# Performance work log

Hardware: AMD Instinct MI355X
Metric: run time of the kernel (lower is better)

Reference implementation:

```python
import jax, jax.numpy as jnp
import numpy as np

B_GRAPHS = 256      # graphs per batch
NPG = 256           # nodes per graph
EXTENT = 32.0       # coordinate extent
K1 = 5              # kernel size per dim
KK = K1 * K1        # 25 weight matrices (dim=2)


def _cartesian(pos, row, col, ev):
    # pseudo-coords: relative cartesian, globally rescaled into [0,1]
    d = pos[col] - pos[row]                                   # [E,2]
    m = jnp.max(jnp.where(ev[:, None] > 0, jnp.abs(d), 0.0))
    return d / (2.0 * m + 1e-12) + 0.5


def _spline_conv(x, row, col, pseudo, ev, W, root, bias, n):
    # degree-1 open B-spline basis, 4 nonzero corners per edge (dim=2)
    v = pseudo * (K1 - 1)
    i0 = jnp.clip(jnp.floor(v), 0, K1 - 2).astype(jnp.int32)  # [E,2]
    f = v - i0
    xin = x[col]                                              # [E,Fin] gather
    acc = jnp.zeros((n * KK, x.shape[1]), x.dtype)
    for sx in (0, 1):
        for sy in (0, 1):
            idx = (i0[:, 0] + sx) * K1 + (i0[:, 1] + sy)      # flat kernel id
            wx = f[:, 0] if sx else 1.0 - f[:, 0]
            wy = f[:, 1] if sy else 1.0 - f[:, 1]
            b = wx * wy * ev
            acc = acc.at[row * KK + idx].add(b[:, None] * xin)
    acc = acc.reshape(n, KK, x.shape[1])                      # [n,25,Fin]
    deg = jax.ops.segment_sum(ev, row, num_segments=n)
    out = jnp.einsum('nki,kio->no', acc, W) / jnp.maximum(deg, 1.0)[:, None]
    return out + x @ root + bias


def _grid_pool(x, pos, row, col, ev, nv, size):
    g = int(EXTENT // size)
    c = jnp.clip(jnp.floor(pos / size).astype(jnp.int32), 0, g - 1)
    cluster = (jnp.arange(x.shape[0], dtype=jnp.int32) * 0)  # placeholder
    cell = c[:, 0] * g + c[:, 1]
    nb = x.shape[0] // 1  # nodes
    # batch id of each node = node's graph; recover from fixed layout
    # (cluster id = graph * g*g + cell)
    per_graph = nb // B_GRAPHS
    gb = jnp.arange(nb, dtype=jnp.int32) // per_graph
    cluster = gb * (g * g) + cell
    Nc = B_GRAPHS * g * g
    seg = jnp.where(nv > 0, cluster, Nc)                      # invalid -> dummy
    xm = jax.ops.segment_max(jnp.where(nv[:, None] > 0, x, -jnp.inf), seg,
                             num_segments=Nc + 1)[:Nc]
    cnt = jax.ops.segment_sum(nv, seg, num_segments=Nc + 1)[:Nc]
    nv2 = (cnt > 0).astype(x.dtype)
    x2 = jnp.where(nv2[:, None] > 0, xm, 0.0)
    pos2 = jax.ops.segment_sum(pos * nv[:, None], seg, num_segments=Nc + 1)[:Nc]
    pos2 = pos2 / jnp.maximum(cnt, 1.0)[:, None]
    batch2 = jnp.arange(Nc, dtype=jnp.int32) // (g * g)
    # remap + coalesce edges (drop self-loops and duplicates, fixed shapes)
    r2 = cluster[row]
    c2 = cluster[col]
    ev2 = (ev > 0) & (r2 != c2)
    key = jnp.where(ev2, r2 * Nc + c2, Nc * Nc)
    order = jnp.argsort(key)
    skey = key[order]
    dup = jnp.concatenate([jnp.zeros((1,), bool), skey[1:] == skey[:-1]])
    ev3 = ((skey < Nc * Nc) & ~dup).astype(x.dtype)
    return x2, pos2, r2[order], c2[order], ev3, batch2, nv2


def _forward(x, position, edge_index, batch, W1, root1, b1, W2, root2, b2,
             W3, root3, b3, fc_w, fc_b):
    row, col = edge_index[0], edge_index[1]
    E, N = row.shape[0], x.shape[0]
    ev = jnp.ones((E,), x.dtype)
    nv = jnp.ones((N,), x.dtype)
    ps = _cartesian(position, row, col, ev)
    h = jax.nn.elu(_spline_conv(x, row, col, ps, ev, W1, root1, b1, N))
    h, pos, row, col, ev, batch2, nv = _grid_pool(h, position, row, col, ev, nv, 4.0)
    ps = _cartesian(pos, row, col, ev)
    h = jax.nn.elu(_spline_conv(h, row, col, ps, ev, W2, root2, b2, h.shape[0]))
    h, pos, row, col, ev, batch2, nv = _grid_pool(h, pos, row, col, ev, nv, 8.0)
    ps = _cartesian(pos, row, col, ev)
    h = jax.nn.elu(_spline_conv(h, row, col, ps, ev, W3, root3, b3, h.shape[0]))
    # scatter_mean over graphs (only non-empty clusters count)
    gsum = jax.ops.segment_sum(h * nv[:, None], batch2, num_segments=B_GRAPHS)
    gcnt = jax.ops.segment_sum(nv, batch2, num_segments=B_GRAPHS)
    gfeat = gsum / jnp.maximum(gcnt, 1.0)[:, None]
    # dropout is identity in eval mode
    logits = gfeat @ fc_w + fc_b
    return jax.nn.log_softmax(logits, axis=1)


def setup_inputs() -> dict:
    DEG = 16
    N = B_GRAPHS * NPG
    E = N * DEG
    key = jax.random.key(0)
    ks = jax.random.split(key, 14)
    x = jax.random.uniform(ks[0], (N, 1), jnp.float32)
    position = jax.random.uniform(ks[1], (N, 2), jnp.float32) * EXTENT
    src = jax.random.randint(ks[2], (E,), 0, N, dtype=jnp.int32)
    tgt = (src // NPG) * NPG + jax.random.randint(ks[3], (E,), 0, NPG, dtype=jnp.int32)
    edge_index = jnp.stack([tgt, src])  # row = target, col = source
    batch = jnp.arange(N, dtype=jnp.int32) // NPG
    s = 0.1
    W1 = jax.random.normal(ks[4], (KK, 1, 32), jnp.float32) * s
    root1 = jax.random.normal(ks[5], (1, 32), jnp.float32) * s
    b1 = jnp.zeros((32,), jnp.float32)
    W2 = jax.random.normal(ks[6], (KK, 32, 64), jnp.float32) * s
    root2 = jax.random.normal(ks[7], (32, 64), jnp.float32) * s
    b2 = jnp.zeros((64,), jnp.float32)
    W3 = jax.random.normal(ks[8], (KK, 64, 128), jnp.float32) * s
    root3 = jax.random.normal(ks[9], (64, 128), jnp.float32) * s
    b3 = jnp.zeros((128,), jnp.float32)
    fc_w = jax.random.normal(ks[10], (128, 10), jnp.float32) * s
    fc_b = jnp.zeros((10,), jnp.float32)
    return dict(x=x, position=position, edge_index=edge_index, batch=batch,
                W1=W1, root1=root1, b1=b1, W2=W2, root2=root2, b2=b2,
                W3=W3, root3=root3, b3=b3, fc_w=fc_w, fc_b=fc_b)


def reference(x, position, edge_index, batch, W1, root1, b1, W2, root2, b2,
              W3, root3, b3, fc_w, fc_b):
    return _forward(x, position, edge_index, batch, W1, root1, b1,
                    W2, root2, b2, W3, root3, b3, fc_w, fc_b)
```

## Files before the change

kernel.cpp:

```cpp
#include <hip/hip_runtime.h>
#include <math.h>

constexpr int NN  = 65536;
constexpr int EE  = 1048576;
constexpr int NG  = 256;
constexpr int NC1 = 16384;
constexpr int NC2 = 4096;
constexpr int EPB = EE / 256;

constexpr size_t O_SCAL  = 0;
constexpr size_t O_GTOT  = 256;
constexpr size_t O_CNT2  = O_GTOT + 1024;
constexpr size_t O_PS2   = O_CNT2 + (size_t)NC2*4;
constexpr size_t Z_END   = O_PS2  + (size_t)NC2*8;
constexpr size_t O_XM2   = Z_END;
constexpr size_t O_GOFF  = O_XM2  + (size_t)NC2*64*4;
constexpr size_t O_BB    = O_GOFF + 1280;
constexpr size_t O_BE    = O_BB   + (size_t)256*256*4;
constexpr size_t O_XP1   = O_BE   + (size_t)EE*2;
constexpr size_t O_POS1  = O_XP1  + (size_t)NC1*32*4;
constexpr size_t O_NV1   = O_POS1 + (size_t)NC1*8;
constexpr size_t O_ADJ2  = O_NV1  + (size_t)NC1*4;
constexpr size_t O_OFF2S = O_ADJ2 + (size_t)NG*4096;
constexpr size_t O_DEG2I = O_OFF2S+ (size_t)NC1*4;
constexpr size_t O_CL2   = O_DEG2I+ (size_t)NC1*4;
constexpr size_t O_XP2   = O_CL2  + (size_t)NC1*4;
constexpr size_t O_POS2  = O_XP2  + (size_t)NC2*64*4;
constexpr size_t O_NV2   = O_POS2 + (size_t)NC2*8;
constexpr size_t O_ADJ3  = O_NV2  + (size_t)NC2*4;
constexpr size_t O_OFF3S = O_ADJ3 + (size_t)NG*256;
constexpr size_t O_DEG3I = O_OFF3S+ (size_t)NC2*4;
constexpr size_t O_H3    = O_DEG3I+ (size_t)NC2*4;
constexpr size_t O_W2Q   = O_H3   + (size_t)NC2*128*4;
constexpr size_t O_W3Q   = O_W2Q  + 102400;
constexpr size_t O_R2T   = O_W3Q  + 409600;
constexpr size_t O_R3T   = O_R2T  + 8192;

typedef __fp16   pk16x2 __attribute__((ext_vector_type(2)));
typedef _Float16 h16x2  __attribute__((ext_vector_type(2)));

__device__ __forceinline__ float eluf(float x){ return x > 0.f ? x : expm1f(x); }

__device__ __forceinline__ void atomic_max_pos(float* a, float v){
    atomicMax((unsigned int*)a, __float_as_uint(v));
}
__device__ __forceinline__ void atomic_max_f32(float* a, float v){
    unsigned int b = __float_as_uint(v);
    if (b & 0x80000000u) atomicMin((unsigned int*)a, b);
    else                 atomicMax((int*)a, (int)b);
}

__device__ __forceinline__ unsigned int pack2(float a, float b){
    pk16x2 h = __builtin_amdgcn_cvt_pkrtz(a, b);
    return __builtin_bit_cast(unsigned int, h);
}
__device__ __forceinline__ unsigned short f2h(float v){
    pk16x2 h = __builtin_amdgcn_cvt_pkrtz(v, v);
    return (unsigned short)(__builtin_bit_cast(unsigned int, h) & 0xFFFFu);
}
__device__ __forceinline__ float dot2u(unsigned int a, unsigned int b, float c){
#if __has_builtin(__builtin_amdgcn_fdot2)
    return __builtin_amdgcn_fdot2(__builtin_bit_cast(h16x2, a),
                                  __builtin_bit_cast(h16x2, b), c, false);
#else
    h16x2 ha = __builtin_bit_cast(h16x2, a), hb = __builtin_bit_cast(h16x2, b);
    return c + (float)ha[0]*(float)hb[0] + (float)ha[1]*(float)hb[1];
#endif
}

struct Crn { int ix, iy; float fx, fy; };
__device__ __forceinline__ Crn mk_corners(float dx, float dy, float m){
    float inv = 1.0f / (2.0f*m + 1e-12f);
    float vx = (dx*inv + 0.5f) * 4.0f;
    float vy = (dy*inv + 0.5f) * 4.0f;
    Crn c;
    c.ix = min(max((int)floorf(vx), 0), 3);
    c.iy = min(max((int)floorf(vy), 0), 3);
    c.fx = vx - (float)c.ix;
    c.fy = vy - (float)c.iy;
    return c;
}

#define BLOCK_MAX_AND_ATOMIC(val, dst)                                   \
    {   __shared__ float _s[256];                                        \
        _s[threadIdx.x] = (val); __syncthreads();                        \
        for (int _w = 128; _w > 0; _w >>= 1){                            \
            if (threadIdx.x < _w)                                        \
                _s[threadIdx.x] = fmaxf(_s[threadIdx.x], _s[threadIdx.x+_w]); \
            __syncthreads();                                             \
        }                                                                \
        if (threadIdx.x == 0) atomic_max_pos((dst), _s[0]); }

__global__ __launch_bounds__(256) void k_prep(
        const float* __restrict__ W2, const float* __restrict__ W3,
        const float* __restrict__ root2, const float* __restrict__ root3,
        unsigned short* __restrict__ w2q, unsigned short* __restrict__ w3q,
        float* __restrict__ r2t, float* __restrict__ r3t){
    int idx = blockIdx.x*256 + threadIdx.x;
    if (idx < 51200){
        int k = idx >> 6, o = idx & 63;
        w2q[(size_t)((k>>3)*64 + o)*8 + (k&7)] = f2h(W2[idx]);
    }
    int i3 = idx - 51200;
    if (i3 >= 0 && i3 < 204800){
        int k = i3 >> 7, o = i3 & 127;
        w3q[(size_t)((k>>3)*128 + o)*8 + (k&7)] = f2h(W3[i3]);
    }
    int ir2 = idx - 256000;
    if (ir2 >= 0 && ir2 < 2048){
        int i = ir2 >> 6, o = ir2 & 63;
        r2t[o*32 + i] = root2[ir2];
    }
    int ir3 = idx - 258048;
    if (ir3 >= 0 && ir3 < 8192){
        int i = ir3 >> 7, o = ir3 & 127;
        r3t[o*64 + i] = root3[ir3];
    }
}

__global__ __launch_bounds__(256) void k_pass1(const int* __restrict__ ei,
                                               const float* __restrict__ pos,
                                               float* m1, int* gtot, int* bb){
    __shared__ int h[256];
    h[threadIdx.x] = 0; __syncthreads();
    int base = blockIdx.x * EPB;
    float loc = 0.f;
    for (int i = threadIdx.x; i < EPB; i += 256){
        int e = base + i;
        int r = ei[e], c = ei[EE + e];
        float dx = pos[2*c]   - pos[2*r];
        float dy = pos[2*c+1] - pos[2*r+1];
        loc = fmaxf(loc, fmaxf(fabsf(dx), fabsf(dy)));
        atomicAdd(&h[r >> 8], 1);
    }
    __syncthreads();
    bb[blockIdx.x*256 + threadIdx.x] = atomicAdd(&gtot[threadIdx.x], h[threadIdx.x]);
    BLOCK_MAX_AND_ATOMIC(loc, m1);
}

__global__ void k_gscan(const int* __restrict__ gtot, int* goff){
    __shared__ int s[256];
    int t = threadIdx.x;
    int v0 = gtot[t];
    s[t] = v0; __syncthreads();
    for (int d = 1; d < 256; d <<= 1){
        int u = (t >= d) ? s[t-d] : 0;
        __syncthreads();
        s[t] += u;
        __syncthreads();
    }
    goff[t] = s[t] - v0;
    if (t == 255) goff[256] = s[t];
}

__global__ __launch_bounds__(256) void k_pass2(const int* __restrict__ ei,
                                               const int* __restrict__ goff,
                                               const int* __restrict__ bb,
                                               unsigned short* __restrict__ be){
    __shared__ int cur[256];
    cur[threadIdx.x] = 0; __syncthreads();
    int base = blockIdx.x * EPB;
    for (int i = threadIdx.x; i < EPB; i += 256){
        int e = base + i;
        int r = ei[e], c = ei[EE + e];
        int g = r >> 8;
        int l = atomicAdd(&cur[g], 1);
        be[goff[g] + bb[blockIdx.x*256 + g] + l] =
            (unsigned short)((r & 255) | ((c & 255) << 8));
    }
}

__global__ __launch_bounds__(256) void k_graph1(
        const unsigned short* __restrict__ be, const int* __restrict__ goff,
        const float* __restrict__ pos, const float* __restrict__ x,
        const float* __restrict__ m1p, const float* __restrict__ W1,
        const float* __restrict__ root1, const float* __restrict__ b1,
        float* __restrict__ xp1, float* __restrict__ pos1g, float* __restrict__ nv1,
        unsigned char* __restrict__ adj2b, int* __restrict__ off2s,
        int* __restrict__ deg2i, float* m2p){
    __shared__ float acc[256*25];
    __shared__ float posx[256], posy[256], xL[256];
    __shared__ int   cl1L[256], degL[256];
    __shared__ float sW[800];
    __shared__ unsigned int bitL[128];
    __shared__ float xmL[64*32];
    __shared__ int   cntL[64];
    __shared__ float psx[64], psy[64];
    __shared__ float p1x[64], p1y[64];
    __shared__ int   rpre[64];

    int t = threadIdx.x, g = blockIdx.x;
    for (int i = t; i < 800; i += 256) sW[i] = W1[i];
    for (int i = t; i < 6400; i += 256) acc[i] = 0.f;
    posx[t] = pos[2*(g*256 + t)];
    posy[t] = pos[2*(g*256 + t) + 1];
    xL[t]   = x[g*256 + t];
    degL[t] = 0;
    if (t < 128) bitL[t] = 0u;
    if (t < 64){ cntL[t] = 0; psx[t] = 0.f; psy[t] = 0.f; }
    for (int i = t; i < 2048; i += 256) xmL[i] = -INFINITY;
    {
        int cx = min(max((int)floorf(posx[t]*0.25f), 0), 7);
        int cy = min(max((int)floorf(posy[t]*0.25f), 0), 7);
        cl1L[t] = cx*8 + cy;
    }
    __syncthreads();

    float mm = *m1p;
    int e1 = goff[g+1];
    for (int p = goff[g] + t; p < e1; p += 256){
        unsigned int b = be[p];
        int rl = b & 255, cl = (b >> 8) & 255;
        float dx = posx[cl] - posx[rl], dy = posy[cl] - posy[rl];
        Crn cr = mk_corners(dx, dy, mm);
        float xin = xL[cl];
        int ab = rl*25 + cr.ix*5 + cr.iy;
        atomicAdd(&acc[ab],   (1.f-cr.fx)*(1.f-cr.fy)*xin);
        atomicAdd(&acc[ab+1], (1.f-cr.fx)*cr.fy*xin);
        atomicAdd(&acc[ab+5], cr.fx*(1.f-cr.fy)*xin);
        atomicAdd(&acc[ab+6], cr.fx*cr.fy*xin);
        atomicAdd(&degL[rl], 1);
        int r2 = cl1L[rl], c2 = cl1L[cl];
        if (r2 != c2){
            int bit = r2*64 + c2;
            atomicOr(&bitL[bit >> 5], 1u << (bit & 31));
        }
    }
    __syncthreads();

    {
        float inv = 1.f / fmaxf((float)degL[t], 1.f);
        float xr  = xL[t];
        int   cl  = cl1L[t];
        atomicAdd(&cntL[cl], 1);
        atomicAdd(&psx[cl], posx[t]);
        atomicAdd(&psy[cl], posy[t]);
        for (int o = 0; o < 32; o++){
            float s = 0.f;
            #pragma unroll
            for (int k = 0; k < 25; k++) s += acc[t*25 + k]*sW[k*32 + o];
            float out = eluf(s*inv + xr*root1[o] + b1[o]);
            atomic_max_f32(&xmL[cl*32 + o], out);
        }
    }
    __syncthreads();

    if (t < 64){
        float cnt = (float)cntL[t];
        float inv = 1.f / fmaxf(cnt, 1.f);
        p1x[t] = psx[t]*inv; p1y[t] = psy[t]*inv;
        pos1g[2*(g*64 + t)]     = p1x[t];
        pos1g[2*(g*64 + t) + 1] = p1y[t];
        nv1[g*64 + t] = (cnt > 0.f) ? 1.f : 0.f;
    }
    __syncthreads();
    for (int i = t; i < 2048; i += 256){
        int c = i >> 5;
        xp1[g*2048 + i] = (cntL[c] > 0) ? xmL[i] : 0.f;
    }

    if (t < 64) rpre[t] = __popc(bitL[2*t]) + __popc(bitL[2*t+1]);
    __syncthreads();
    for (int d = 1; d < 64; d <<= 1){
        int v = 0;
        if (t < 64 && t >= d) v = rpre[t-d];
        __syncthreads();
        if (t < 64) rpre[t] += v;
        __syncthreads();
    }
    float m2loc = 0.f;
    if (t < 64){
        unsigned int w0 = bitL[2*t], w1 = bitL[2*t+1];
        int dg = __popc(w0) + __popc(w1);
        int baseo = rpre[t] - dg;
        off2s[g*64 + t] = g*4096 + baseo;
        deg2i[g*64 + t] = dg;
        int j = g*4096 + baseo;
        float rx = p1x[t], ry = p1y[t];
        while (w0){
            int b = __ffs(w0) - 1; w0 &= w0 - 1;
            adj2b[j++] = (unsigned char)b;
            m2loc = fmaxf(m2loc, fmaxf(fabsf(p1x[b]-rx), fabsf(p1y[b]-ry)));
        }
        while (w1){
            int b = __ffs(w1) - 1; w1 &= w1 - 1;
            int c = 32 + b;
            adj2b[j++] = (unsigned char)c;
            m2loc = fmaxf(m2loc, fmaxf(fabsf(p1x[c]-rx), fabsf(p1y[c]-ry)));
        }
    }
    BLOCK_MAX_AND_ATOMIC(m2loc, m2p);
}

__global__ __launch_bounds__(512) void k_conv2(
        const int* __restrict__ off2s, const int* __restrict__ deg2i,
        const unsigned char* __restrict__ adj2b, const float* __restrict__ pos1g,
        const float* __restrict__ m2p, const float* __restrict__ xp1,
        const unsigned short* __restrict__ w2q, const float* __restrict__ r2t,
        const float* __restrict__ b2, const float* __restrict__ nv1,
        int* __restrict__ cl2, float* cnt2, float* ps2, float* xm2){
    __shared__ __align__(16) float am[16*800];
    __shared__ __align__(16) float xpL[64*32];
    __shared__ float p1x[64], p1y[64];
    int t = threadIdx.x;
    int g = blockIdx.x >> 2, sub = blockIdx.x & 3;
    for (int i = t; i < 12800; i += 512) am[i] = 0.f;
    for (int i = t; i < 2048; i += 512) xpL[i] = xp1[g*2048 + i];
    if (t < 64){ p1x[t] = pos1g[2*(g*64+t)]; p1y[t] = pos1g[2*(g*64+t)+1]; }
    __syncthreads();
    int grp = t >> 5, lane = t & 31;
    {
        int rl = sub*16 + grp;
        int r  = g*64 + rl;
        int s0 = off2s[r], n = deg2i[r];
        float rx = p1x[rl], ry = p1y[rl];
        float mm = *m2p;
        float* a = &am[grp*800];
        for (int j = 0; j < n; ++j){
            int cLoc = adj2b[s0 + j];
            float dx = p1x[cLoc] - rx, dy = p1y[cLoc] - ry;
            Crn cr = mk_corners(dx, dy, mm);
            float xin = xpL[cLoc*32 + lane];
            int b = (cr.ix*5 + cr.iy)*32 + lane;
            a[b]     += (1.f-cr.fx)*(1.f-cr.fy)*xin;
            a[b+32]  += (1.f-cr.fx)*cr.fy*xin;
            a[b+160] += cr.fx*(1.f-cr.fy)*xin;
            a[b+192] += cr.fx*cr.fy*xin;
        }
    }
    __syncthreads();
    unsigned int* amu = (unsigned int*)am;
    {
        unsigned int tmpv[13];
        #pragma unroll
        for (int j = 0; j < 13; j++){
            int i = t + j*512;
            if (i < 6400){
                int row = i/400, kp = i - row*400;
                tmpv[j] = pack2(am[row*800 + 2*kp], am[row*800 + 2*kp + 1]);
            }
        }
        __syncthreads();
        #pragma unroll
        for (int j = 0; j < 13; j++){
            int i = t + j*512;
            if (i < 6400) amu[i] = tmpv[j];
        }
        __syncthreads();
    }
    int o = t & 63, mg = t >> 6;
    const unsigned int* a0 = amu + mg*400;
    const unsigned int* a1 = amu + (mg+8)*400;
    const uint4* wq = (const uint4*)w2q;
    float sA0=0.f, sA1=0.f, sB0=0.f, sB1=0.f;
    for (int kp8 = 0; kp8 < 100; kp8++){
        uint4 wv = wq[kp8*64 + o];
        uint4 av = *(const uint4*)(a0 + kp8*4);
        uint4 bv = *(const uint4*)(a1 + kp8*4);
        sA0 = dot2u(av.x, wv.x, sA0); sA1 = dot2u(av.y, wv.y, sA1);
        sA0 = dot2u(av.z, wv.z, sA0); sA1 = dot2u(av.w, wv.w, sA1);
        sB0 = dot2u(bv.x, wv.x, sB0); sB1 = dot2u(bv.y, wv.y, sB1);
        sB0 = dot2u(bv.z, wv.z, sB0); sB1 = dot2u(bv.w, wv.w, sB1);
    }
    float sAB[2] = {sA0 + sA1, sB0 + sB1};
    #pragma unroll
    for (int h = 0; h < 2; ++h){
        int rl = sub*16 + mg + h*8;
        int rr = g*64 + rl;
        float s  = sAB[h];
        float dg = fmaxf((float)deg2i[rr], 1.f);
        float rt = 0.f;
        #pragma unroll
        for (int i = 0; i < 32; i += 4){
            float4 rv = *(const float4*)&r2t[o*32 + i];
            float4 xv = *(const float4*)&xpL[rl*32 + i];
            rt += rv.x*xv.x + rv.y*xv.y + rv.z*xv.z + rv.w*xv.w;
        }
        float val = eluf(s/dg + rt + b2[o]);
        float px = p1x[rl], py = p1y[rl];
        int cx = min(max((int)floorf(px*0.125f), 0), 3);
        int cy = min(max((int)floorf(py*0.125f), 0), 3);
        int cl = g*16 + cx*4 + cy;
        if (o == 0) cl2[rr] = cl;
        if (nv1[rr] > 0.f){
            if (o == 0){
                atomicAdd(&cnt2[cl], 1.f);
                atomicAdd(&ps2[2*cl],   px);
                atomicAdd(&ps2[2*cl+1], py);
            }
            atomic_max_f32(&xm2[cl*64 + o], val);
        }
    }
}

__global__ __launch_bounds__(256) void k_lvl3(
        const int* __restrict__ off2s, const int* __restrict__ deg2i,
        const unsigned char* __restrict__ adj2b, const int* __restrict__ cl2,
        const float* __restrict__ cnt2, const float* __restrict__ ps2,
        const float* __restrict__ xm2,
        float* __restrict__ xp2, float* __restrict__ pos2g, float* __restrict__ nv2,
        unsigned char* __restrict__ adj3b, int* __restrict__ off3s,
        int* __restrict__ deg3i, float* m3p){
    __shared__ int cl2L[64];
    __shared__ unsigned int bit3[8];
    __shared__ float p2x[16], p2y[16];
    __shared__ int rpre[16];
    int t = threadIdx.x, g = blockIdx.x;
    if (t < 64) cl2L[t] = cl2[g*64 + t] & 15;
    if (t < 8)  bit3[t] = 0u;
    if (t < 16){
        float cnt = cnt2[g*16 + t];
        float inv = 1.f / fmaxf(cnt, 1.f);
        p2x[t] = ps2[2*(g*16+t)]*inv;
        p2y[t] = ps2[2*(g*16+t)+1]*inv;
        pos2g[2*(g*16+t)]   = p2x[t];
        pos2g[2*(g*16+t)+1] = p2y[t];
        nv2[g*16 + t] = (cnt > 0.f) ? 1.f : 0.f;
    }
    for (int i = t; i < 1024; i += 256){
        int c = i >> 6;
        xp2[g*1024 + i] = (cnt2[g*16 + c] > 0.f) ? xm2[g*1024 + i] : 0.f;
    }
    __syncthreads();
    if (t < 64){
        int s0 = off2s[g*64 + t], n = deg2i[g*64 + t];
        int r3 = cl2L[t];
        for (int j = 0; j < n; ++j){
            int c3 = cl2L[adj2b[s0 + j]];
            if (r3 != c3){
                int bit = r3*16 + c3;
                atomicOr(&bit3[bit >> 5], 1u << (bit & 31));
            }
        }
    }
    __syncthreads();
    if (t < 16)
        rpre[t] = __popc((bit3[t >> 1] >> ((t & 1)*16)) & 0xFFFFu);
    __syncthreads();
    for (int d = 1; d < 16; d <<= 1){
        int v = 0;
        if (t < 16 && t >= d) v = rpre[t-d];
        __syncthreads();
        if (t < 16) rpre[t] += v;
        __syncthreads();
    }
    float m3loc = 0.f;
    if (t < 16){
        unsigned int w = (bit3[t >> 1] >> ((t & 1)*16)) & 0xFFFFu;
        int dg = __popc(w);
        int baseo = rpre[t] - dg;
        off3s[g*16 + t] = g*256 + baseo;
        deg3i[g*16 + t] = dg;
        int j = g*256 + baseo;
        float rx = p2x[t], ry = p2y[t];
        while (w){
            int b = __ffs(w) - 1; w &= w - 1;
            adj3b[j++] = (unsigned char)b;
            m3loc = fmaxf(m3loc, fmaxf(fabsf(p2x[b]-rx), fabsf(p2y[b]-ry)));
        }
    }
    BLOCK_MAX_AND_ATOMIC(m3loc, m3p);
}

__global__ __launch_bounds__(512) void k_conv3(
        const int* __restrict__ off3s, const int* __restrict__ deg3i,
        const unsigned char* __restrict__ adj3b, const float* __restrict__ pos2g,
        const float* __restrict__ m3p, const float* __restrict__ xp2,
        const unsigned short* __restrict__ w3q, const float* __restrict__ r3t,
        const float* __restrict__ b3, float* __restrict__ h3){
    __shared__ __align__(16) float am[8*1600];
    __shared__ __align__(16) float xpL[16*64];
    __shared__ float p2x[16], p2y[16];
    int t = threadIdx.x;
    int g = blockIdx.x >> 1, sub = blockIdx.x & 1;
    for (int i = t; i < 12800; i += 512) am[i] = 0.f;
    for (int i = t; i < 1024; i += 512) xpL[i] = xp2[g*1024 + i];
    if (t < 16){ p2x[t] = pos2g[2*(g*16+t)]; p2y[t] = pos2g[2*(g*16+t)+1]; }
    __syncthreads();
    int grp = t >> 6, lane = t & 63;
    {
        int rl = sub*8 + grp;
        int r  = g*16 + rl;
        int s0 = off3s[r], n = deg3i[r];
        float rx = p2x[rl], ry = p2y[rl];
        float mm = *m3p;
        float* a = &am[grp*1600];
        for (int j = 0; j < n; ++j){
            int cLoc = adj3b[s0 + j];
            float dx = p2x[cLoc] - rx, dy = p2y[cLoc] - ry;
            Crn cr = mk_corners(dx, dy, mm);
            float xin = xpL[cLoc*64 + lane];
            int b = (cr.ix*5 + cr.iy)*64 + lane;
            a[b]     += (1.f-cr.fx)*(1.f-cr.fy)*xin;
            a[b+64]  += (1.f-cr.fx)*cr.fy*xin;
            a[b+320] += cr.fx*(1.f-cr.fy)*xin;
            a[b+384] += cr.fx*cr.fy*xin;
        }
    }
    __syncthreads();
    unsigned int* amu = (unsigned int*)am;
    {
        unsigned int tmpv[13];
        #pragma unroll
        for (int j = 0; j < 13; j++){
            int i = t + j*512;
            if (i < 6400){
                int row = i/800, kp = i - row*800;
                tmpv[j] = pack2(am[row*1600 + 2*kp], am[row*1600 + 2*kp + 1]);
            }
        }
        __syncthreads();
        #pragma unroll
        for (int j = 0; j < 13; j++){
            int i = t + j*512;
            if (i < 6400) amu[i] = tmpv[j];
        }
        __syncthreads();
    }
    int o = t & 127, mg = t >> 7;
    const unsigned int* a0 = amu + mg*800;
    const unsigned int* a1 = amu + (mg+4)*800;
    const uint4* wq = (const uint4*)w3q;
    float sA0=0.f, sA1=0.f, sB0=0.f, sB1=0.f;
    for (int kp8 = 0; kp8 < 200; kp8++){
        uint4 wv = wq[kp8*128 + o];
        uint4 av = *(const uint4*)(a0 + kp8*4);
        uint4 bv = *(const uint4*)(a1 + kp8*4);
        sA0 = dot2u(av.x, wv.x, sA0); sA1 = dot2u(av.y, wv.y, sA1);
        sA0 = dot2u(av.z, wv.z, sA0); sA1 = dot2u(av.w, wv.w, sA1);
        sB0 = dot2u(bv.x, wv.x, sB0); sB1 = dot2u(bv.y, wv.y, sB1);
        sB0 = dot2u(bv.z, wv.z, sB0); sB1 = dot2u(bv.w, wv.w, sB1);
    }
    float sAB[2] = {sA0 + sA1, sB0 + sB1};
    #pragma unroll
    for (int h = 0; h < 2; ++h){
        int rl = sub*8 + mg + h*4;
        int rr = g*16 + rl;
        float s  = sAB[h];
        float dg = fmaxf((float)deg3i[rr], 1.f);
        float rt = 0.f;
        #pragma unroll
        for (int i = 0; i < 64; i += 4){
            float4 rv = *(const float4*)&r3t[o*64 + i];
            float4 xv = *(const float4*)&xpL[rl*64 + i];
            rt += rv.x*xv.x + rv.y*xv.y + rv.z*xv.z + rv.w*xv.w;
        }
        h3[rr*128 + o] = eluf(s/dg + rt + b3[o]);
    }
}

__global__ void k_readout(const float* __restrict__ h3, const float* __restrict__ nv2,
                          const float* __restrict__ fcw, const float* __restrict__ fcb,
                          float* out){
    int g = blockIdx.x, t = threadIdx.x;
    __shared__ float gf[128];
    __shared__ float lg[10];
    __shared__ float lse;
    float s = 0.f, cnt = 0.f;
    for (int j = 0; j < 16; j++){
        int c = g*16 + j;
        float nv = nv2[c];
        s += h3[c*128 + t] * nv;
        cnt += nv;
    }
    gf[t] = s / fmaxf(cnt, 1.f);
    __syncthreads();
    if (t < 10){
        float l = fcb[t];
        for (int f = 0; f < 128; f++) l += gf[f]*fcw[f*10 + t];
        lg[t] = l;
    }
    __syncthreads();
    if (t == 0){
        float mx = -INFINITY;
        for (int o = 0; o < 10; o++) mx = fmaxf(mx, lg[o]);
        float ss = 0.f;
        for (int o = 0; o < 10; o++) ss += expf(lg[o] - mx);
        lse = mx + logf(ss);
    }
    __syncthreads();
    if (t < 10) out[g*10 + t] = lg[t] - lse;
}

extern "C" void kernel_launch(void* const* d_in, const int* in_sizes, int n_in,
                              void* d_out, int out_size, void* d_ws, size_t ws_size,
                              hipStream_t stream){
    const float* x     = (const float*)d_in[0];
    const float* posi  = (const float*)d_in[1];
    const int*   ei    = (const int*)  d_in[2];
    const float* W1    = (const float*)d_in[4];
    const float* root1 = (const float*)d_in[5];
    const float* b1    = (const float*)d_in[6];
    const float* W2    = (const float*)d_in[7];
    const float* root2 = (const float*)d_in[8];
    const float* b2    = (const float*)d_in[9];
    const float* W3    = (const float*)d_in[10];
    const float* root3 = (const float*)d_in[11];
    const float* b3    = (const float*)d_in[12];
    const float* fcw   = (const float*)d_in[13];
    const float* fcb   = (const float*)d_in[14];
    float* out = (float*)d_out;

    char* ws = (char*)d_ws;
    float*          m1    = (float*)(ws + O_SCAL);
    float*          m2    = m1 + 1;
    float*          m3    = m1 + 2;
    int*            gtot  = (int*)  (ws + O_GTOT);
    float*          cnt2  = (float*)(ws + O_CNT2);
    float*          ps2   = (float*)(ws + O_PS2);
    float*          xm2   = (float*)(ws + O_XM2);
    int*            goff  = (int*)  (ws + O_GOFF);
    int*            bb    = (int*)  (ws + O_BB);
    unsigned short* be    = (unsigned short*)(ws + O_BE);
    float*          xp1   = (float*)(ws + O_XP1);
    float*          pos1g = (float*)(ws + O_POS1);
    float*          nv1   = (float*)(ws + O_NV1);
    unsigned char*  adj2b = (unsigned char*)(ws + O_ADJ2);
    int*            off2s = (int*)  (ws + O_OFF2S);
    int*            deg2i = (int*)  (ws + O_DEG2I);
    int*            cl2   = (int*)  (ws + O_CL2);
    float*          xp2   = (float*)(ws + O_XP2);
    float*          pos2g = (float*)(ws + O_POS2);
    float*          nv2   = (float*)(ws + O_NV2);
    unsigned char*  adj3b = (unsigned char*)(ws + O_ADJ3);
    int*            off3s = (int*)  (ws + O_OFF3S);
    int*            deg3i = (int*)  (ws + O_DEG3I);
    float*          h3    = (float*)(ws + O_H3);
    unsigned short* w2q   = (unsigned short*)(ws + O_W2Q);
    unsigned short* w3q   = (unsigned short*)(ws + O_W3Q);
    float*          r2t   = (float*)(ws + O_R2T);
    float*          r3t   = (float*)(ws + O_R3T);

    hipMemsetAsync(ws, 0, Z_END, stream);
    hipMemsetAsync(xm2, 0xFF, (size_t)NC2*64*4, stream);

    k_prep<<<1040, 256, 0, stream>>>(W2, W3, root2, root3, w2q, w3q, r2t, r3t);
    k_pass1<<<256, 256, 0, stream>>>(ei, posi, m1, gtot, bb);
    k_gscan<<<1, 256, 0, stream>>>(gtot, goff);
    k_pass2<<<256, 256, 0, stream>>>(ei, goff, bb, be);

    k_graph1<<<NG, 256, 0, stream>>>(be, goff, posi, x, m1, W1, root1, b1,
                                     xp1, pos1g, nv1, adj2b, off2s, deg2i, m2);

    k_conv2<<<NC1/16, 512, 0, stream>>>(off2s, deg2i, adj2b, pos1g, m2, xp1,
                                        w2q, r2t, b2, nv1, cl2, cnt2, ps2, xm2);

    k_lvl3<<<NG, 256, 0, stream>>>(off2s, deg2i, adj2b, cl2, cnt2, ps2, xm2,
                                   xp2, pos2g, nv2, adj3b, off3s, deg3i, m3);

    k_conv3<<<NC2/8, 512, 0, stream>>>(off3s, deg3i, adj3b, pos2g, m3, xp2,
                                       w3q, r3t, b3, h3);

    k_readout<<<256, 128, 0, stream>>>(h3, nv2, fcw, fcb, out);
}
```

Baseline: 300.6 us.

## Fuse prep into pass1, widen graph1 to 1024 threads, register-accumulate conv basis

Merges the weight-prep kernel into k_pass1 as extra blocks, removing one launch. k_graph1 now runs with 1024 threads, so edge processing and the per-node output loop (split four ways per node) get more parallelism, and its final max uses a small shared reduction. In k_conv2 and k_conv3 the per-lane spline accumulation now uses 25 registers with a dense hat-function basis instead of shared-memory scatter. The fp16 packing is done through a lane shuffle, which drops the shared-memory zeroing and repack passes. The dense basis does more FLOPs per edge and raises register pressure.

Result: faster. 290.2 us (-3.5%).

```diff
diff --git a/kernel.cpp b/kernel.cpp
--- a/kernel.cpp
+++ b/kernel.cpp
@@ -91,37 +91,37 @@
         }                                                                \
         if (threadIdx.x == 0) atomic_max_pos((dst), _s[0]); }
 
-__global__ __launch_bounds__(256) void k_prep(
+__global__ __launch_bounds__(256) void k_pass1(
+        const int* __restrict__ ei, const float* __restrict__ pos,
+        float* m1, int* gtot, int* bb,
         const float* __restrict__ W2, const float* __restrict__ W3,
         const float* __restrict__ root2, const float* __restrict__ root3,
         unsigned short* __restrict__ w2q, unsigned short* __restrict__ w3q,
         float* __restrict__ r2t, float* __restrict__ r3t){
-    int idx = blockIdx.x*256 + threadIdx.x;
-    if (idx < 51200){
-        int k = idx >> 6, o = idx & 63;
-        w2q[(size_t)((k>>3)*64 + o)*8 + (k&7)] = f2h(W2[idx]);
-    }
-    int i3 = idx - 51200;
-    if (i3 >= 0 && i3 < 204800){
-        int k = i3 >> 7, o = i3 & 127;
-        w3q[(size_t)((k>>3)*128 + o)*8 + (k&7)] = f2h(W3[i3]);
-    }
-    int ir2 = idx - 256000;
-    if (ir2 >= 0 && ir2 < 2048){
-        int i = ir2 >> 6, o = ir2 & 63;
-        r2t[o*32 + i] = root2[ir2];
-    }
-    int ir3 = idx - 258048;
-    if (ir3 >= 0 && ir3 < 8192){
-        int i = ir3 >> 7, o = ir3 & 127;
-        r3t[o*64 + i] = root3[ir3];
-    }
-}
-
-__global__ __launch_bounds__(256) void k_pass1(const int* __restrict__ ei,
-                                               const float* __restrict__ pos,
-                                               float* m1, int* gtot, int* bb){
     __shared__ int h[256];
+    if (blockIdx.x >= 256){
+        int idx = (blockIdx.x - 256)*256 + threadIdx.x;
+        if (idx < 51200){
+            int k = idx >> 6, o = idx & 63;
+            w2q[(size_t)((k>>3)*64 + o)*8 + (k&7)] = f2h(W2[idx]);
+        }
+        int i3 = idx - 51200;
+        if (i3 >= 0 && i3 < 204800){
+            int k = i3 >> 7, o = i3 & 127;
+            w3q[(size_t)((k>>3)*128 + o)*8 + (k&7)] = f2h(W3[i3]);
+        }
+        int ir2 = idx - 256000;
+        if (ir2 >= 0 && ir2 < 2048){
+            int i = ir2 >> 6, o = ir2 & 63;
+            r2t[o*32 + i] = root2[ir2];
+        }
+        int ir3 = idx - 258048;
+        if (ir3 >= 0 && ir3 < 8192){
+            int i = ir3 >> 7, o = ir3 & 127;
+            r3t[o*64 + i] = root3[ir3];
+        }
+        return;
+    }
     h[threadIdx.x] = 0; __syncthreads();
     int base = blockIdx.x * EPB;
     float loc = 0.f;
@@ -170,7 +170,7 @@
     }
 }
 
-__global__ __launch_bounds__(256) void k_graph1(
+__global__ __launch_bounds__(1024) void k_graph1(
         const unsigned short* __restrict__ be, const int* __restrict__ goff,
         const float* __restrict__ pos, const float* __restrict__ x,
         const float* __restrict__ m1p, const float* __restrict__ W1,
@@ -188,27 +188,28 @@
     __shared__ float psx[64], psy[64];
     __shared__ float p1x[64], p1y[64];
     __shared__ int   rpre[64];
+    __shared__ float mred[64];
 
     int t = threadIdx.x, g = blockIdx.x;
-    for (int i = t; i < 800; i += 256) sW[i] = W1[i];
-    for (int i = t; i < 6400; i += 256) acc[i] = 0.f;
-    posx[t] = pos[2*(g*256 + t)];
-    posy[t] = pos[2*(g*256 + t) + 1];
-    xL[t]   = x[g*256 + t];
-    degL[t] = 0;
+    if (t < 800) sW[t] = W1[t];
+    for (int i = t; i < 6400; i += 1024) acc[i] = 0.f;
+    if (t < 256){
+        float px = pos[2*(g*256 + t)], py = pos[2*(g*256 + t) + 1];
+        posx[t] = px; posy[t] = py;
+        xL[t]   = x[g*256 + t];
+        degL[t] = 0;
+        int cx = min(max((int)floorf(px*0.25f), 0), 7);
+        int cy = min(max((int)floorf(py*0.25f), 0), 7);
+        cl1L[t] = cx*8 + cy;
+    }
     if (t < 128) bitL[t] = 0u;
     if (t < 64){ cntL[t] = 0; psx[t] = 0.f; psy[t] = 0.f; }
-    for (int i = t; i < 2048; i += 256) xmL[i] = -INFINITY;
-    {
-        int cx = min(max((int)floorf(posx[t]*0.25f), 0), 7);
-        int cy = min(max((int)floorf(posy[t]*0.25f), 0), 7);
-        cl1L[t] = cx*8 + cy;
-    }
+    for (int i = t; i < 2048; i += 1024) xmL[i] = -INFINITY;
     __syncthreads();
 
     float mm = *m1p;
     int e1 = goff[g+1];
-    for (int p = goff[g] + t; p < e1; p += 256){
+    for (int p = goff[g] + t; p < e1; p += 1024){
         unsigned int b = be[p];
         int rl = b & 255, cl = (b >> 8) & 255;
         float dx = posx[cl] - posx[rl], dy = posy[cl] - posy[rl];
@@ -229,16 +230,24 @@
     __syncthreads();
 
     {
-        float inv = 1.f / fmaxf((float)degL[t], 1.f);
-        float xr  = xL[t];
-        int   cl  = cl1L[t];
-        atomicAdd(&cntL[cl], 1);
-        atomicAdd(&psx[cl], posx[t]);
-        atomicAdd(&psy[cl], posy[t]);
-        for (int o = 0; o < 32; o++){
+        int n = t >> 2, q = t & 3;
+        float accR[25];
+        #pragma unroll
+        for (int k = 0; k < 25; k++) accR[k] = acc[n*25 + k];
+        float inv = 1.f / fmaxf((float)degL[n], 1.f);
+        float xr  = xL[n];
+        int   cl  = cl1L[n];
+        if (q == 0){
+            atomicAdd(&cntL[cl], 1);
+            atomicAdd(&psx[cl], posx[n]);
+            atomicAdd(&psy[cl], posy[n]);
+        }
+        #pragma unroll
+        for (int oo = 0; oo < 8; oo++){
+            int o = q*8 + oo;
             float s = 0.f;
             #pragma unroll
-            for (int k = 0; k < 25; k++) s += acc[t*25 + k]*sW[k*32 + o];
+            for (int k = 0; k < 25; k++) s += accR[k]*sW[k*32 + o];
             float out = eluf(s*inv + xr*root1[o] + b1[o]);
             atomic_max_f32(&xmL[cl*32 + o], out);
         }
@@ -254,7 +263,7 @@
         nv1[g*64 + t] = (cnt > 0.f) ? 1.f : 0.f;
     }
     __syncthreads();
-    for (int i = t; i < 2048; i += 256){
+    for (int i = t; i < 2048; i += 1024){
         int c = i >> 5;
         xp1[g*2048 + i] = (cntL[c] > 0) ? xmL[i] : 0.f;
     }
@@ -288,8 +297,14 @@
             adj2b[j++] = (unsigned char)c;
             m2loc = fmaxf(m2loc, fmaxf(fabsf(p1x[c]-rx), fabsf(p1y[c]-ry)));
         }
-    }
-    BLOCK_MAX_AND_ATOMIC(m2loc, m2p);
+        mred[t] = m2loc;
+    }
+    __syncthreads();
+    if (t == 0){
+        float v = mred[0];
+        for (int i = 1; i < 64; i++) v = fmaxf(v, mred[i]);
+        atomic_max_pos(m2p, v);
+    }
 }
 
 __global__ __launch_bounds__(512) void k_conv2(
@@ -299,12 +314,11 @@
         const unsigned short* __restrict__ w2q, const float* __restrict__ r2t,
         const float* __restrict__ b2, const float* __restrict__ nv1,
         int* __restrict__ cl2, float* cnt2, float* ps2, float* xm2){
-    __shared__ __align__(16) float am[16*800];
+    __shared__ __align__(16) unsigned int amu[16*400];
     __shared__ __align__(16) float xpL[64*32];
     __shared__ float p1x[64], p1y[64];
     int t = threadIdx.x;
     int g = blockIdx.x >> 2, sub = blockIdx.x & 3;
-    for (int i = t; i < 12800; i += 512) am[i] = 0.f;
     for (int i = t; i < 2048; i += 512) xpL[i] = xp1[g*2048 + i];
     if (t < 64){ p1x[t] = pos1g[2*(g*64+t)]; p1y[t] = pos1g[2*(g*64+t)+1]; }
     __syncthreads();
@@ -315,39 +329,35 @@
         int s0 = off2s[r], n = deg2i[r];
         float rx = p1x[rl], ry = p1y[rl];
         float mm = *m2p;
-        float* a = &am[grp*800];
+        float inv = 1.0f / (2.0f*mm + 1e-12f);
+        float acc[25];
+        #pragma unroll
+        for (int k = 0; k < 25; k++) acc[k] = 0.f;
         for (int j = 0; j < n; ++j){
             int cLoc = adj2b[s0 + j];
-            float dx = p1x[cLoc] - rx, dy = p1y[cLoc] - ry;
-            Crn cr = mk_corners(dx, dy, mm);
+            float vx = ((p1x[cLoc] - rx)*inv + 0.5f)*4.0f;
+            float vy = ((p1y[cLoc] - ry)*inv + 0.5f)*4.0f;
             float xin = xpL[cLoc*32 + lane];
-            int b = (cr.ix*5 + cr.iy)*32 + lane;
-            a[b]     += (1.f-cr.fx)*(1.f-cr.fy)*xin;
-            a[b+32]  += (1.f-cr.fx)*cr.fy*xin;
-            a[b+160] += cr.fx*(1.f-cr.fy)*xin;
-            a[b+192] += cr.fx*cr.fy*xin;
-        }
-    }
-    __syncthreads();
-    unsigned int* amu = (unsigned int*)am;
-    {
-        unsigned int tmpv[13];
-        #pragma unroll
-        for (int j = 0; j < 13; j++){
-            int i = t + j*512;
-            if (i < 6400){
-                int row = i/400, kp = i - row*400;
-                tmpv[j] = pack2(am[row*800 + 2*kp], am[row*800 + 2*kp + 1]);
+            float wxx[5], wy[5];
+            #pragma unroll
+            for (int k = 0; k < 5; k++){
+                wxx[k] = fmaxf(0.f, 1.f - fabsf(vx - (float)k)) * xin;
+                wy[k]  = fmaxf(0.f, 1.f - fabsf(vy - (float)k));
             }
-        }
-        __syncthreads();
-        #pragma unroll
-        for (int j = 0; j < 13; j++){
-            int i = t + j*512;
-            if (i < 6400) amu[i] = tmpv[j];
-        }
-        __syncthreads();
-    }
+            #pragma unroll
+            for (int kx = 0; kx < 5; kx++)
+                #pragma unroll
+                for (int ky = 0; ky < 5; ky++)
+                    acc[kx*5+ky] = fmaf(wxx[kx], wy[ky], acc[kx*5+ky]);
+        }
+        unsigned int* dst = &amu[grp*400];
+        #pragma unroll
+        for (int k = 0; k < 25; k++){
+            float other = __shfl_xor(acc[k], 1, 64);
+            if (!(lane & 1)) dst[k*16 + (lane >> 1)] = pack2(acc[k], other);
+        }
+    }
+    __syncthreads();
     int o = t & 63, mg = t >> 6;
     const unsigned int* a0 = amu + mg*400;
     const unsigned int* a1 = amu + (mg+8)*400;
@@ -468,12 +478,11 @@
         const float* __restrict__ m3p, const float* __restrict__ xp2,
         const unsigned short* __restrict__ w3q, const float* __restrict__ r3t,
         const float* __restrict__ b3, float* __restrict__ h3){
-    __shared__ __align__(16) float am[8*1600];
+    __shared__ __align__(16) unsigned int amu[8*800];
     __shared__ __align__(16) float xpL[16*64];
     __shared__ float p2x[16], p2y[16];
     int t = threadIdx.x;
     int g = blockIdx.x >> 1, sub = blockIdx.x & 1;
-    for (int i = t; i < 12800; i += 512) am[i] = 0.f;
     for (int i = t; i < 1024; i += 512) xpL[i] = xp2[g*1024 + i];
     if (t < 16){ p2x[t] = pos2g[2*(g*16+t)]; p2y[t] = pos2g[2*(g*16+t)+1]; }
     __syncthreads();
@@ -484,39 +493,35 @@
         int s0 = off3s[r], n = deg3i[r];
         float rx = p2x[rl], ry = p2y[rl];
         float mm = *m3p;
-        float* a = &am[grp*1600];
+        float inv = 1.0f / (2.0f*mm + 1e-12f);
+        float acc[25];
+        #pragma unroll
+        for (int k = 0; k < 25; k++) acc[k] = 0.f;
         for (int j = 0; j < n; ++j){
             int cLoc = adj3b[s0 + j];
-            float dx = p2x[cLoc] - rx, dy = p2y[cLoc] - ry;
-            Crn cr = mk_corners(dx, dy, mm);
+            float vx = ((p2x[cLoc] - rx)*inv + 0.5f)*4.0f;
+            float vy = ((p2y[cLoc] - ry)*inv + 0.5f)*4.0f;
             float xin = xpL[cLoc*64 + lane];
-            int b = (cr.ix*5 + cr.iy)*64 + lane;
-            a[b]     += (1.f-cr.fx)*(1.f-cr.fy)*xin;
-            a[b+64]  += (1.f-cr.fx)*cr.fy*xin;
-            a[b+320] += cr.fx*(1.f-cr.fy)*xin;
-            a[b+384] += cr.fx*cr.fy*xin;
-        }
-    }
-    __syncthreads();
-    unsigned int* amu = (unsigned int*)am;
-    {
-        unsigned int tmpv[13];
-        #pragma unroll
-        for (int j = 0; j < 13; j++){
-            int i = t + j*512;
-            if (i < 6400){
-                int row = i/800, kp = i - row*800;
-                tmpv[j] = pack2(am[row*1600 + 2*kp], am[row*1600 + 2*kp + 1]);
+            float wxx[5], wy[5];
+            #pragma unroll
+            for (int k = 0; k < 5; k++){
+                wxx[k] = fmaxf(0.f, 1.f - fabsf(vx - (float)k)) * xin;
+                wy[k]  = fmaxf(0.f, 1.f - fabsf(vy - (float)k));
             }
-        }
-        __syncthreads();
-        #pragma unroll
-        for (int j = 0; j < 13; j++){
-            int i = t + j*512;
-            if (i < 6400) amu[i] = tmpv[j];
-        }
-        __syncthreads();
-    }
+            #pragma unroll
+            for (int kx = 0; kx < 5; kx++)
+                #pragma unroll
+                for (int ky = 0; ky < 5; ky++)
+                    acc[kx*5+ky] = fmaf(wxx[kx], wy[ky], acc[kx*5+ky]);
+        }
+        unsigned int* dst = &amu[grp*800];
+        #pragma unroll
+        for (int k = 0; k < 25; k++){
+            float other = __shfl_xor(acc[k], 1, 64);
+            if (!(lane & 1)) dst[k*32 + (lane >> 1)] = pack2(acc[k], other);
+        }
+    }
+    __syncthreads();
     int o = t & 127, mg = t >> 7;
     const unsigned int* a0 = amu + mg*800;
     const unsigned int* a1 = amu + (mg+4)*800;
@@ -634,13 +639,13 @@
     hipMemsetAsync(ws, 0, Z_END, stream);
     hipMemsetAsync(xm2, 0xFF, (size_t)NC2*64*4, stream);
 
-    k_prep<<<1040, 256, 0, stream>>>(W2, W3, root2, root3, w2q, w3q, r2t, r3t);
-    k_pass1<<<256, 256, 0, stream>>>(ei, posi, m1, gtot, bb);
+    k_pass1<<<256 + 1040, 256, 0, stream>>>(ei, posi, m1, gtot, bb,
+                                            W2, W3, root2, root3, w2q, w3q, r2t, r3t);
     k_gscan<<<1, 256, 0, stream>>>(gtot, goff);
     k_pass2<<<256, 256, 0, stream>>>(ei, goff, bb, be);
 
-    k_graph1<<<NG, 256, 0, stream>>>(be, goff, posi, x, m1, W1, root1, b1,
-                                     xp1, pos1g, nv1, adj2b, off2s, deg2i, m2);
+    k_graph1<<<NG, 1024, 0, stream>>>(be, goff, posi, x, m1, W1, root1, b1,
+                                      xp1, pos1g, nv1, adj2b, off2s, deg2i, m2);
 
     k_conv2<<<NC1/16, 512, 0, stream>>>(off2s, deg2i, adj2b, pos1g, m2, xp1,
                                         w2q, r2t, b2, nv1, cl2, cnt2, ps2, xm2);
```
